# Kernel optimization log

Hardware: AMD Instinct MI355X
Metric: run time of the kernel (lower is better)

The kernel has to match this reference:

```python
import jax, jax.numpy as jnp
import numpy as np

B, N, DIM = 2, 2048, 512
HEADS, DIM_HEAD = 8, 64
INNER = HEADS * DIM_HEAD  # 512
SCALE = DIM_HEAD ** -0.5


def setup_inputs() -> dict:
    key = jax.random.key(0)
    k1, k2, k3, k4, k5 = jax.random.split(key, 5)
    s = 0.02
    return {
        "x1": jax.random.normal(k1, (B, N, DIM), jnp.float32),
        "x2": jax.random.normal(k2, (B, N, DIM), jnp.float32),
        "W_qk": jax.random.normal(k3, (DIM, 2 * INNER), jnp.float32) * s,
        "W_v": jax.random.normal(k4, (DIM, INNER), jnp.float32) * s,
        "W_out": jax.random.normal(k5, (INNER, DIM), jnp.float32) * s,
        "b_out": jnp.zeros((DIM,), jnp.float32),
    }


def _split_heads(t):
    # [b, n, h*d] -> [b, h, n, d]
    b, n, _ = t.shape
    return t.reshape(b, n, HEADS, DIM_HEAD).transpose(0, 2, 1, 3)


def reference(x1, x2, W_qk, W_v, W_out, b_out):
    # to_qk(x1) -> chunk into k, v ; to_v(x2) -> q  (names in orig are swapped)
    kv = x1 @ W_qk                      # [b, n1, 2*inner]
    k, v = jnp.split(kv, 2, axis=-1)
    q = x2 @ W_v                        # [b, n2, inner]
    q, k, v = _split_heads(q), _split_heads(k), _split_heads(v)  # [b,h,n,d]
    dots = jnp.einsum("bhid,bhjd->bhij", q, k) * SCALE  # [b,h,n2,n1]
    attn = jax.nn.softmax(dots, axis=-1)
    out = jnp.einsum("bhij,bhjd->bhid", attn, v)         # [b,h,n2,d]
    out = out.transpose(0, 2, 1, 3).reshape(out.shape[0], out.shape[2], INNER)
    return out @ W_out + b_out          # [b, n2, dim]
```

## Files before the change

kernel.cpp:

```cpp
#include <hip/hip_runtime.h>

typedef short bf16x8 __attribute__((ext_vector_type(8)));
typedef short bf16x4 __attribute__((ext_vector_type(4)));
typedef float f32x4 __attribute__((ext_vector_type(4)));
typedef float f32x16 __attribute__((ext_vector_type(16)));
typedef unsigned short u16;
typedef unsigned int u32;
typedef u16 u16x8 __attribute__((ext_vector_type(8)));
typedef u16 u16x4 __attribute__((ext_vector_type(4)));

#define DEV __device__ __forceinline__

DEV u16 f2bf(float f) {
  unsigned u = __float_as_uint(f);
  u += 0x7fff + ((u >> 16) & 1);
  return (u16)(u >> 16);
}

DEV int pkbf(float lo, float hi) {
  return __builtin_amdgcn_perm(__float_as_uint(hi) + 0x8000u,
                               __float_as_uint(lo) + 0x8000u, 0x07060302u);
}

#define MFMA16(a, b, c) __builtin_amdgcn_mfma_f32_16x16x32_bf16(a, b, c, 0, 0, 0)
#define MFMA3216(a, b, c) __builtin_amdgcn_mfma_f32_32x32x16_bf16(a, b, c, 0, 0, 0)

#if __has_builtin(__builtin_amdgcn_mfma_f32_32x32x8bf16_1k)
#define HAVE_PV8 1
#define PVMFMA(a, b, c) __builtin_amdgcn_mfma_f32_32x32x8bf16_1k(a, b, c, 0, 0, 0)
#else
#define HAVE_PV8 0
#endif

#if __has_builtin(__builtin_amdgcn_exp2f)
#define QSCALE 0.18033688011112042f
#define EXPFN(x) __builtin_amdgcn_exp2f(x)
#else
#define QSCALE 0.125f
#define EXPFN(x) __expf(x)
#endif

#define GLD16(gp, lp)                                                     \
  __builtin_amdgcn_global_load_lds(                                       \
      (const __attribute__((address_space(1))) u32*)(gp),                 \
      (__attribute__((address_space(3))) u32*)(lp), 16, 0, 0)

__global__ __launch_bounds__(256) void wprep(
    const float* __restrict__ Wqk, const float* __restrict__ Wv,
    const float* __restrict__ Wout,
    u16* __restrict__ WqkT, u16* __restrict__ WvT, u16* __restrict__ WoutT) {
  __shared__ float tf[32][33];
  int bx = blockIdx.x, t = threadIdx.x;
  const float* src; u16* dst; int Ncols; int id;
  if (bx < 512)      { id = bx;       src = Wqk;  dst = WqkT;  Ncols = 1024; }
  else if (bx < 768) { id = bx - 512; src = Wv;   dst = WvT;   Ncols = 512; }
  else               { id = bx - 768; src = Wout; dst = WoutT; Ncols = 512; }
  int tilesPerRow = Ncols >> 5;
  int tr = id / tilesPerRow, tc = id % tilesPerRow;
  int r0 = tr * 32, c0 = tc * 32;
  {
    int r = t >> 3, c4 = (t & 7) * 4;
    float4 v = *(const float4*)(src + (long)(r0 + r) * Ncols + c0 + c4);
    tf[r][c4] = v.x; tf[r][c4 + 1] = v.y; tf[r][c4 + 2] = v.z; tf[r][c4 + 3] = v.w;
  }
  __syncthreads();
  {
    int c = t >> 3, r4 = (t & 7) * 4;
    u16x4 o;
    o[0] = f2bf(tf[r4][c]); o[1] = f2bf(tf[r4 + 1][c]);
    o[2] = f2bf(tf[r4 + 2][c]); o[3] = f2bf(tf[r4 + 3][c]);
    *(u16x4*)(dst + (long)(c0 + c) * 512 + r0 + r4) = o;
  }
}

__global__ __launch_bounds__(256) void qkv_gemm(
    const float* __restrict__ x1, const float* __restrict__ x2,
    const u16* __restrict__ WqkT, const u16* __restrict__ WvT,
    u16* __restrict__ out_q, u16* __restrict__ out_k, u16* __restrict__ out_vt) {
  __shared__ u16 sA[2][128 * 40];
  __shared__ u16 sB[2][64 * 40];
  int bx = blockIdx.x, t = threadIdx.x;
  bool isQ = bx < 256;
  int bx2 = isQ ? bx : bx - 256;
  const float* Ap = isQ ? x2 : x1;
  const u16* BT = isQ ? WvT : WqkT;
  int m0 = (bx2 & 31) * 128, n0 = (bx2 >> 5) * 64;
  int w = t >> 6, l = t & 63, lm = l & 15, lq = l >> 4;

  f32x4 zero = {0.f, 0.f, 0.f, 0.f};
  f32x4 acc[2][4];
#pragma unroll
  for (int i = 0; i < 2; ++i)
#pragma unroll
    for (int j = 0; j < 4; ++j) acc[i][j] = zero;

  int sm = t >> 2;
  int skc = (t & 3) * 8;
  const float* gAf = Ap + (long)(m0 + sm) * 512 + skc;
  const u16* gB = BT + (long)(n0 + sm) * 512 + skc;

  auto loadA = [&](int kt, int rows) {
    long off = (long)rows * 512 + kt * 32;
    float4 f0 = *(const float4*)(gAf + off);
    float4 f1 = *(const float4*)(gAf + off + 4);
    bf16x8 o;
    o[0] = (short)f2bf(f0.x); o[1] = (short)f2bf(f0.y);
    o[2] = (short)f2bf(f0.z); o[3] = (short)f2bf(f0.w);
    o[4] = (short)f2bf(f1.x); o[5] = (short)f2bf(f1.y);
    o[6] = (short)f2bf(f1.z); o[7] = (short)f2bf(f1.w);
    return o;
  };

  bf16x8 a0 = loadA(0, 0);
  bf16x8 a1 = loadA(0, 64);
  bf16x8 b0 = *(const bf16x8*)(gB);
  *(bf16x8*)(sA[0] + sm * 40 + skc) = a0;
  *(bf16x8*)(sA[0] + (sm + 64) * 40 + skc) = a1;
  *(bf16x8*)(sB[0] + sm * 40 + skc) = b0;
  __syncthreads();

  for (int kt = 0; kt < 16; ++kt) {
    int cur = kt & 1;
    if (kt < 15) {
      a0 = loadA(kt + 1, 0);
      a1 = loadA(kt + 1, 64);
      b0 = *(const bf16x8*)(gB + (kt + 1) * 32);
    }
    bf16x8 af[2], bfr[4];
    af[0] = *(const bf16x8*)(sA[cur] + (w * 32 + lm) * 40 + lq * 8);
    af[1] = *(const bf16x8*)(sA[cur] + (w * 32 + 16 + lm) * 40 + lq * 8);
#pragma unroll
    for (int s = 0; s < 4; ++s)
      bfr[s] = *(const bf16x8*)(sB[cur] + (s * 16 + lm) * 40 + lq * 8);
#pragma unroll
    for (int ms = 0; ms < 2; ++ms)
#pragma unroll
      for (int s = 0; s < 4; ++s)
        acc[ms][s] = MFMA16(af[ms], bfr[s], acc[ms][s]);
    if (kt < 15) {
      int nxt = 1 - cur;
      *(bf16x8*)(sA[nxt] + sm * 40 + skc) = a0;
      *(bf16x8*)(sA[nxt] + (sm + 64) * 40 + skc) = a1;
      *(bf16x8*)(sB[nxt] + sm * 40 + skc) = b0;
    }
    __syncthreads();
  }

#pragma unroll
  for (int ms = 0; ms < 2; ++ms) {
    int gmBase = m0 + w * 32 + ms * 16 + lq * 4;
#pragma unroll
    for (int s = 0; s < 4; ++s) {
      int gc = n0 + s * 16 + lm;
      int b = gmBase >> 11, n = gmBase & 2047;
      if (isQ) {
#pragma unroll
        for (int r = 0; r < 4; ++r)
          out_q[(((long)(b << 3) + (gc >> 6)) * 2048 + n + r) * 64 + (gc & 63)] =
              f2bf(acc[ms][s][r] * QSCALE);
      } else if (gc < 512) {
#pragma unroll
        for (int r = 0; r < 4; ++r)
          out_k[(((long)(b << 3) + (gc >> 6)) * 2048 + n + r) * 64 + (gc & 63)] =
              f2bf(acc[ms][s][r]);
      } else {
        int c = gc - 512, h = c >> 6, d = c & 63;
        u16x4 vv;
#pragma unroll
        for (int r = 0; r < 4; ++r) vv[r] = f2bf(acc[ms][s][r]);
        *(u16x4*)(out_vt + (((long)(b << 3) + h) * 64 + d) * 2048 + n) = vv;
      }
    }
  }
}

__global__ __launch_bounds__(256, 4) void attn(
    const u16* __restrict__ Q, const u16* __restrict__ K,
    const u16* __restrict__ Vt, u16* __restrict__ O) {
  int id = blockIdx.x;
  int bh = id & 15, qt = id >> 4;
  int b = bh >> 3, h = bh & 7;
  const u16* Kh = K + (long)bh * 2048 * 64;
  const u16* Vh = Vt + (long)bh * 64 * 2048;
  int t = threadIdx.x, w = t >> 6, lane = t & 63, ln = lane & 31, hi = lane >> 5;
  int g = w & 1, kh = w >> 1;

  __shared__ u16 smem[2][2][4096];
  u16* sKh = smem[0][kh];
  u16* sVh = smem[1][kh];

  bf16x8 qf[4];
  {
    const u16* qp = Q + (long)bh * 2048 * 64 + (long)(qt * 64 + g * 32 + ln) * 64 + hi * 8;
#pragma unroll
    for (int dc = 0; dc < 4; ++dc) qf[dc] = *(const bf16x8*)(qp + dc * 16);
  }

  f32x16 accO[2];
#pragma unroll
  for (int dt = 0; dt < 2; ++dt)
#pragma unroll
    for (int i = 0; i < 16; ++i) accO[dt][i] = 0.f;
  float dacc = 0.f;

  int lrow = lane >> 3;
  int swz = ((lane & 7) ^ lrow) * 8;
  const u16* gKl = Kh + (long)(kh * 1024 + g * 32 + lrow) * 64 + swz;
  const u16* gVl = Vh + (long)(g * 32 + lrow) * 2048 + kh * 1024 + swz;

  auto stage = [&](int jt) {
    const u16* gk = gKl + (long)jt * 4096;
    const u16* gv = gVl + jt * 64;
#pragma unroll
    for (int i = 0; i < 4; ++i) {
      GLD16(gk + i * 512, sKh + (g * 32 + i * 8) * 64);
      GLD16(gv + (long)i * 16384, sVh + (g * 32 + i * 8) * 64);
    }
  };

  stage(0);
  __syncthreads();

  int swl = ln & 7;
  for (int jt = 0; jt < 16; ++jt) {
#pragma unroll
    for (int kt2 = 0; kt2 < 2; ++kt2) {
      int rowK = (kt2 * 32 + ln) * 64;
      f32x16 st1, st2;
#pragma unroll
      for (int i = 0; i < 16; ++i) { st1[i] = 0.f; st2[i] = 0.f; }
      bf16x8 kf0 = *(const bf16x8*)(sKh + rowK + ((0 * 2 + hi) ^ swl) * 8);
      bf16x8 kf1 = *(const bf16x8*)(sKh + rowK + ((1 * 2 + hi) ^ swl) * 8);
      bf16x8 kf2 = *(const bf16x8*)(sKh + rowK + ((2 * 2 + hi) ^ swl) * 8);
      bf16x8 kf3 = *(const bf16x8*)(sKh + rowK + ((3 * 2 + hi) ^ swl) * 8);
      st1 = MFMA3216(kf0, qf[0], st1);
      st2 = MFMA3216(kf1, qf[1], st2);
      st1 = MFMA3216(kf2, qf[2], st1);
      st2 = MFMA3216(kf3, qf[3], st2);
      float p[16];
#pragma unroll
      for (int i = 0; i < 16; ++i) {
        float e = EXPFN(st1[i] + st2[i]);
        p[i] = e;
        dacc += e;
      }
#if HAVE_PV8
#pragma unroll
      for (int c = 0; c < 4; ++c) {
        union { int2 i2; bf16x4 v; } u;
        u.i2.x = pkbf(p[c * 4 + 0], p[c * 4 + 1]);
        u.i2.y = pkbf(p[c * 4 + 2], p[c * 4 + 3]);
#pragma unroll
        for (int dt = 0; dt < 2; ++dt) {
          bf16x4 vf = *(const bf16x4*)(sVh + (dt * 32 + ln) * 64 +
                                       (((kt2 * 4 + c) ^ swl) * 8) + hi * 4);
          accO[dt] = PVMFMA(vf, u.v, accO[dt]);
        }
      }
#else
#pragma unroll
      for (int c2 = 0; c2 < 2; ++c2) {
        int o0x = pkbf(p[c2 * 8 + 0], p[c2 * 8 + 1]);
        int o0y = pkbf(p[c2 * 8 + 2], p[c2 * 8 + 3]);
        int o1x = pkbf(p[c2 * 8 + 4], p[c2 * 8 + 5]);
        int o1y = pkbf(p[c2 * 8 + 6], p[c2 * 8 + 7]);
        int s0x = __shfl_xor(o0x, 32), s0y = __shfl_xor(o0y, 32);
        int s1x = __shfl_xor(o1x, 32), s1y = __shfl_xor(o1y, 32);
        union { int4 i4; bf16x8 v; } u;
        if (hi) { u.i4.x = s1x; u.i4.y = s1y; u.i4.z = o1x; u.i4.w = o1y; }
        else    { u.i4.x = o0x; u.i4.y = o0y; u.i4.z = s0x; u.i4.w = s0y; }
#pragma unroll
        for (int dt = 0; dt < 2; ++dt) {
          bf16x8 vf = *(const bf16x8*)(sVh + (dt * 32 + ln) * 64 +
                                       (((kt2 * 4 + c2 * 2 + hi) ^ swl) * 8));
          accO[dt] = MFMA3216(vf, u.v, accO[dt]);
        }
      }
#endif
    }
    __syncthreads();
    if (jt < 15) {
      stage(jt + 1);
      __syncthreads();
    }
  }

  float* cb = (float*)&smem[0][0][0];
  float* base = cb + g * 2112;
  if (kh == 1) {
#pragma unroll
    for (int dt = 0; dt < 2; ++dt)
#pragma unroll
      for (int i = 0; i < 16; ++i)
        base[(dt * 16 + i) * 64 + hi * 32 + ln] = accO[dt][i];
    base[2048 + hi * 32 + ln] = dacc;
  }
  __syncthreads();
  if (kh == 0) {
#pragma unroll
    for (int dt = 0; dt < 2; ++dt)
#pragma unroll
      for (int i = 0; i < 16; ++i)
        accO[dt][i] += base[(dt * 16 + i) * 64 + hi * 32 + ln];
    dacc += base[2048 + hi * 32 + ln];
    dacc += __shfl_xor(dacc, 32);
    float inv = 1.f / dacc;

    u16* Ob = O + ((long)b * 2048 + qt * 64 + g * 32 + ln) * 512 + h * 64;
#pragma unroll
    for (int dt = 0; dt < 2; ++dt)
#pragma unroll
      for (int gq = 0; gq < 4; ++gq) {
        u16x4 o;
#pragma unroll
        for (int rr = 0; rr < 4; ++rr) o[rr] = f2bf(accO[dt][gq * 4 + rr] * inv);
        *(u16x4*)(Ob + dt * 32 + gq * 8 + hi * 4) = o;
      }
  }
}

__global__ __launch_bounds__(128) void out_gemm(
    const u16* __restrict__ A, const u16* __restrict__ BT,
    float* __restrict__ out_f, const float* __restrict__ bias) {
  __shared__ u16 sA[2][64 * 40];
  __shared__ u16 sB[2][32 * 40];
  int t = threadIdx.x, bx = blockIdx.x;
  int m0 = (bx & 63) * 64, n0 = (bx >> 6) * 32;
  int w = t >> 6, l = t & 63, lm = l & 15, lq = l >> 4;

  f32x4 zero = {0.f, 0.f, 0.f, 0.f};
  f32x4 acc[2][2];
#pragma unroll
  for (int i = 0; i < 2; ++i)
#pragma unroll
    for (int j = 0; j < 2; ++j) acc[i][j] = zero;

  int ar = t >> 1, akc = (t & 1) * 16;
  int br = t >> 2, bkc = (t & 3) * 8;
  const u16* gA = A + (long)(m0 + ar) * 512 + akc;
  const u16* gB = BT + (long)(n0 + br) * 512 + bkc;

  bf16x8 a0 = *(const bf16x8*)(gA);
  bf16x8 a1 = *(const bf16x8*)(gA + 8);
  bf16x8 b0 = *(const bf16x8*)(gB);
  *(bf16x8*)(sA[0] + ar * 40 + akc) = a0;
  *(bf16x8*)(sA[0] + ar * 40 + akc + 8) = a1;
  *(bf16x8*)(sB[0] + br * 40 + bkc) = b0;
  __syncthreads();

  for (int kt = 0; kt < 16; ++kt) {
    int cur = kt & 1;
    if (kt < 15) {
      a0 = *(const bf16x8*)(gA + (kt + 1) * 32);
      a1 = *(const bf16x8*)(gA + (kt + 1) * 32 + 8);
      b0 = *(const bf16x8*)(gB + (kt + 1) * 32);
    }
    bf16x8 af[2], bfr[2];
    af[0] = *(const bf16x8*)(sA[cur] + (w * 32 + lm) * 40 + lq * 8);
    af[1] = *(const bf16x8*)(sA[cur] + (w * 32 + 16 + lm) * 40 + lq * 8);
    bfr[0] = *(const bf16x8*)(sB[cur] + (lm)*40 + lq * 8);
    bfr[1] = *(const bf16x8*)(sB[cur] + (16 + lm) * 40 + lq * 8);
#pragma unroll
    for (int ms = 0; ms < 2; ++ms)
#pragma unroll
      for (int s = 0; s < 2; ++s)
        acc[ms][s] = MFMA16(af[ms], bfr[s], acc[ms][s]);
    if (kt < 15) {
      int nxt = 1 - cur;
      *(bf16x8*)(sA[nxt] + ar * 40 + akc) = a0;
      *(bf16x8*)(sA[nxt] + ar * 40 + akc + 8) = a1;
      *(bf16x8*)(sB[nxt] + br * 40 + bkc) = b0;
    }
    __syncthreads();
  }

#pragma unroll
  for (int ms = 0; ms < 2; ++ms) {
    int gmBase = m0 + w * 32 + ms * 16 + lq * 4;
#pragma unroll
    for (int s = 0; s < 2; ++s) {
      int gc = n0 + s * 16 + lm;
      float bv = bias[gc];
#pragma unroll
      for (int r = 0; r < 4; ++r)
        out_f[(long)(gmBase + r) * 512 + gc] = acc[ms][s][r] + bv;
    }
  }
}

extern "C" void kernel_launch(void* const* d_in, const int* in_sizes, int n_in,
                              void* d_out, int out_size, void* d_ws, size_t ws_size,
                              hipStream_t stream) {
  const float* x1 = (const float*)d_in[0];
  const float* x2 = (const float*)d_in[1];
  const float* Wqk = (const float*)d_in[2];
  const float* Wv = (const float*)d_in[3];
  const float* Wout = (const float*)d_in[4];
  const float* bout = (const float*)d_in[5];
  float* out = (float*)d_out;

  u16* ws = (u16*)d_ws;
  const long SZ = 2097152;
  u16* Qw = ws;
  u16* Kw = ws + SZ;
  u16* Vtw = ws + 2 * SZ;
  u16* Ow = ws + 3 * SZ;
  u16* WqkT = ws + 4 * SZ;
  u16* WvT = WqkT + 524288;
  u16* WoutT = WvT + 262144;

  wprep<<<1024, 256, 0, stream>>>(Wqk, Wv, Wout, WqkT, WvT, WoutT);
  qkv_gemm<<<768, 256, 0, stream>>>(x1, x2, WqkT, WvT, Qw, Kw, Vtw);
  attn<<<512, 256, 0, stream>>>(Qw, Kw, Vtw, Ow);
  out_gemm<<<1024, 128, 0, stream>>>(Ow, WoutT, out, bout);
}
```

Before: 126.8 us.

## Pre-convert activations to bf16 and double-buffer K/V staging in attention

The weight-prep kernel now also converts x1 and x2 to bf16 in separate blocks, so the QKV GEMM loads bf16 directly instead of converting fp32 on every tile load. That removes repeated conversion work across the column-tile blocks that read the same rows. In exchange it adds an extra pass over the activations through workspace memory. The attention kernel now double-buffers its K/V shared-memory tiles, issuing the next tile's async loads before computing on the current one. This drops one barrier per iteration but doubles LDS use, and the occupancy hint falls from 4 to 2 blocks per CU.

```diff
diff --git a/kernel.cpp b/kernel.cpp
--- a/kernel.cpp
+++ b/kernel.cpp
@@ -48,9 +48,24 @@
 __global__ __launch_bounds__(256) void wprep(
     const float* __restrict__ Wqk, const float* __restrict__ Wv,
     const float* __restrict__ Wout,
-    u16* __restrict__ WqkT, u16* __restrict__ WvT, u16* __restrict__ WoutT) {
+    const float* __restrict__ x1, const float* __restrict__ x2,
+    u16* __restrict__ WqkT, u16* __restrict__ WvT, u16* __restrict__ WoutT,
+    u16* __restrict__ x1b, u16* __restrict__ x2b) {
   __shared__ float tf[32][33];
   int bx = blockIdx.x, t = threadIdx.x;
+  if (bx >= 1024) {
+    int id = bx - 1024;
+    const float* src = id < 1024 ? x1 : x2;
+    u16* dst = id < 1024 ? x1b : x2b;
+    long base = (long)(id & 1023) * 2048 + t * 8;
+    float4 f0 = *(const float4*)(src + base);
+    float4 f1 = *(const float4*)(src + base + 4);
+    u16x8 o;
+    o[0] = f2bf(f0.x); o[1] = f2bf(f0.y); o[2] = f2bf(f0.z); o[3] = f2bf(f0.w);
+    o[4] = f2bf(f1.x); o[5] = f2bf(f1.y); o[6] = f2bf(f1.z); o[7] = f2bf(f1.w);
+    *(u16x8*)(dst + base) = o;
+    return;
+  }
   const float* src; u16* dst; int Ncols; int id;
   if (bx < 512)      { id = bx;       src = Wqk;  dst = WqkT;  Ncols = 1024; }
   else if (bx < 768) { id = bx - 512; src = Wv;   dst = WvT;   Ncols = 512; }
@@ -74,7 +89,7 @@
 }
 
 __global__ __launch_bounds__(256) void qkv_gemm(
-    const float* __restrict__ x1, const float* __restrict__ x2,
+    const u16* __restrict__ x1b, const u16* __restrict__ x2b,
     const u16* __restrict__ WqkT, const u16* __restrict__ WvT,
     u16* __restrict__ out_q, u16* __restrict__ out_k, u16* __restrict__ out_vt) {
   __shared__ u16 sA[2][128 * 40];
@@ -82,7 +97,7 @@
   int bx = blockIdx.x, t = threadIdx.x;
   bool isQ = bx < 256;
   int bx2 = isQ ? bx : bx - 256;
-  const float* Ap = isQ ? x2 : x1;
+  const u16* Ap = isQ ? x2b : x1b;
   const u16* BT = isQ ? WvT : WqkT;
   int m0 = (bx2 & 31) * 128, n0 = (bx2 >> 5) * 64;
   int w = t >> 6, l = t & 63, lm = l & 15, lq = l >> 4;
@@ -96,23 +111,11 @@
 
   int sm = t >> 2;
   int skc = (t & 3) * 8;
-  const float* gAf = Ap + (long)(m0 + sm) * 512 + skc;
+  const u16* gA = Ap + (long)(m0 + sm) * 512 + skc;
   const u16* gB = BT + (long)(n0 + sm) * 512 + skc;
 
-  auto loadA = [&](int kt, int rows) {
-    long off = (long)rows * 512 + kt * 32;
-    float4 f0 = *(const float4*)(gAf + off);
-    float4 f1 = *(const float4*)(gAf + off + 4);
-    bf16x8 o;
-    o[0] = (short)f2bf(f0.x); o[1] = (short)f2bf(f0.y);
-    o[2] = (short)f2bf(f0.z); o[3] = (short)f2bf(f0.w);
-    o[4] = (short)f2bf(f1.x); o[5] = (short)f2bf(f1.y);
-    o[6] = (short)f2bf(f1.z); o[7] = (short)f2bf(f1.w);
-    return o;
-  };
-
-  bf16x8 a0 = loadA(0, 0);
-  bf16x8 a1 = loadA(0, 64);
+  bf16x8 a0 = *(const bf16x8*)(gA);
+  bf16x8 a1 = *(const bf16x8*)(gA + 64 * 512);
   bf16x8 b0 = *(const bf16x8*)(gB);
   *(bf16x8*)(sA[0] + sm * 40 + skc) = a0;
   *(bf16x8*)(sA[0] + (sm + 64) * 40 + skc) = a1;
@@ -122,8 +125,8 @@
   for (int kt = 0; kt < 16; ++kt) {
     int cur = kt & 1;
     if (kt < 15) {
-      a0 = loadA(kt + 1, 0);
-      a1 = loadA(kt + 1, 64);
+      a0 = *(const bf16x8*)(gA + (kt + 1) * 32);
+      a1 = *(const bf16x8*)(gA + 64 * 512 + (kt + 1) * 32);
       b0 = *(const bf16x8*)(gB + (kt + 1) * 32);
     }
     bf16x8 af[2], bfr[4];
@@ -174,7 +177,7 @@
   }
 }
 
-__global__ __launch_bounds__(256, 4) void attn(
+__global__ __launch_bounds__(256, 2) void attn(
     const u16* __restrict__ Q, const u16* __restrict__ K,
     const u16* __restrict__ Vt, u16* __restrict__ O) {
   int id = blockIdx.x;
@@ -185,9 +188,7 @@
   int t = threadIdx.x, w = t >> 6, lane = t & 63, ln = lane & 31, hi = lane >> 5;
   int g = w & 1, kh = w >> 1;
 
-  __shared__ u16 smem[2][2][4096];
-  u16* sKh = smem[0][kh];
-  u16* sVh = smem[1][kh];
+  __shared__ u16 smem[2][2][2][4096];
 
   bf16x8 qf[4];
   {
@@ -208,21 +209,27 @@
   const u16* gKl = Kh + (long)(kh * 1024 + g * 32 + lrow) * 64 + swz;
   const u16* gVl = Vh + (long)(g * 32 + lrow) * 2048 + kh * 1024 + swz;
 
-  auto stage = [&](int jt) {
+  auto stage = [&](int jt, int buf) {
+    u16* sK = smem[buf][0][kh];
+    u16* sV = smem[buf][1][kh];
     const u16* gk = gKl + (long)jt * 4096;
     const u16* gv = gVl + jt * 64;
 #pragma unroll
     for (int i = 0; i < 4; ++i) {
-      GLD16(gk + i * 512, sKh + (g * 32 + i * 8) * 64);
-      GLD16(gv + (long)i * 16384, sVh + (g * 32 + i * 8) * 64);
+      GLD16(gk + i * 512, sK + (g * 32 + i * 8) * 64);
+      GLD16(gv + (long)i * 16384, sV + (g * 32 + i * 8) * 64);
     }
   };
 
-  stage(0);
+  stage(0, 0);
   __syncthreads();
 
   int swl = ln & 7;
   for (int jt = 0; jt < 16; ++jt) {
+    int cur = jt & 1;
+    if (jt < 15) stage(jt + 1, cur ^ 1);
+    const u16* sKh = smem[cur][0][kh];
+    const u16* sVh = smem[cur][1][kh];
 #pragma unroll
     for (int kt2 = 0; kt2 < 2; ++kt2) {
       int rowK = (kt2 * 32 + ln) * 64;
@@ -279,13 +286,9 @@
 #endif
     }
     __syncthreads();
-    if (jt < 15) {
-      stage(jt + 1);
-      __syncthreads();
-    }
-  }
-
-  float* cb = (float*)&smem[0][0][0];
+  }
+
+  float* cb = (float*)&smem[0][0][0][0];
   float* base = cb + g * 2112;
   if (kh == 1) {
 #pragma unroll
@@ -408,9 +411,11 @@
   u16* WqkT = ws + 4 * SZ;
   u16* WvT = WqkT + 524288;
   u16* WoutT = WvT + 262144;
-
-  wprep<<<1024, 256, 0, stream>>>(Wqk, Wv, Wout, WqkT, WvT, WoutT);
-  qkv_gemm<<<768, 256, 0, stream>>>(x1, x2, WqkT, WvT, Qw, Kw, Vtw);
+  u16* x1b = WoutT + 262144;
+  u16* x2b = x1b + SZ;
+
+  wprep<<<3072, 256, 0, stream>>>(Wqk, Wv, Wout, x1, x2, WqkT, WvT, WoutT, x1b, x2b);
+  qkv_gemm<<<768, 256, 0, stream>>>(x1b, x2b, WqkT, WvT, Qw, Kw, Vtw);
   attn<<<512, 256, 0, stream>>>(Qw, Kw, Vtw, Ow);
   out_gemm<<<1024, 128, 0, stream>>>(Ow, WoutT, out, bout);
 }
```

After: 126.6 us. No clear change (-0.1%).
